# Kernel tuning notes

Hardware: AMD Instinct MI355X
Metric: run time of the kernel (lower is better)

## Reference

```python
import jax, jax.numpy as jnp
import numpy as np

N = 100000
E = 3200000
IN_F, HID_F, OUT_F = 512, 256, 64
ALPHA = 0.01
K = 10


def setup_inputs() -> dict:
    key = jax.random.key(0)
    ks = jax.random.split(key, 8)
    x = jax.random.normal(ks[0], (N, IN_F), dtype=jnp.float32)
    W1 = jax.random.normal(ks[1], (IN_F, HID_F), dtype=jnp.float32) * (1.0 / np.sqrt(IN_F))
    b1 = jnp.zeros((HID_F,), dtype=jnp.float32)
    W2 = jax.random.normal(ks[2], (HID_F, OUT_F), dtype=jnp.float32) * (1.0 / np.sqrt(HID_F))
    b2 = jnp.zeros((OUT_F,), dtype=jnp.float32)
    row = jax.random.randint(ks[3], (E,), 0, N, dtype=jnp.int32)
    col = jax.random.randint(ks[4], (E,), 0, N, dtype=jnp.int32)
    # normalized-ish positive edge weights
    edge_weight = jax.random.uniform(ks[5], (E,), dtype=jnp.float32) / 32.0
    return {"x": x, "W1": W1, "b1": b1, "W2": W2, "b2": b2,
            "edge_weight": edge_weight, "row": row, "col": col}


def _spmm(row, col, w, h):
    # sparse [N,N] @ dense [N,d]: out[r] += w_e * h[col_e]
    msgs = h[col] * w[:, None]  # [E, d]
    return jax.ops.segment_sum(msgs, row, num_segments=N)


def reference(x, W1, b1, W2, b2, edge_weight, row, col):
    h = jax.nn.relu(x @ W1 + b1)          # linear1 + activation (dropout p=0 -> identity)
    h = h @ W2 + b2                        # linear2
    for _ in range(K):                     # k-step PPR propagation, alpha-blended residual
        h = (1.0 - ALPHA) * _spmm(row, col, edge_weight, h) + ALPHA * h
    return h
```

## Files before the change

kernel.cpp:

```cpp
#include <hip/hip_runtime.h>


#define N_NODES 100000
#define N_EDGES 3200000
#define IN_F    512
#define HID_F   256
#define OUT_F   64
#define NBKT    ((N_NODES + 63) / 64)
#define CAP     4096
#define SBLK    250
#define SCHUNK  12800

typedef short bf16x8 __attribute__((ext_vector_type(8)));
typedef float f32x4  __attribute__((ext_vector_type(4)));

__device__ __forceinline__ unsigned short f2bf(float f) {
    unsigned int u = __float_as_uint(f);
    unsigned int r = (u + 0x7FFFu + ((u >> 16) & 1u)) >> 16;
    return (unsigned short)r;
}
__device__ __forceinline__ float bf2f(unsigned short h) {
    return __uint_as_float(((unsigned int)h) << 16);
}

__global__ void cast_transpose_w1(const float* __restrict__ w, unsigned short* __restrict__ wt) {
    int idx = blockIdx.x * blockDim.x + threadIdx.x;
    if (idx >= IN_F * HID_F) return;
    int k = idx / HID_F, n = idx % HID_F;
    wt[(size_t)n * IN_F + k] = f2bf(w[idx]);
}
__global__ void cast_transpose_w2(const float* __restrict__ w, unsigned short* __restrict__ wt) {
    int idx = blockIdx.x * blockDim.x + threadIdx.x;
    if (idx >= HID_F * OUT_F) return;
    int k = idx / OUT_F, n = idx % OUT_F;
    wt[(size_t)n * HID_F + k] = f2bf(w[idx]);
}

__global__ __launch_bounds__(256) void cast_x(const float* __restrict__ x,
                                              unsigned short* __restrict__ xb) {
    int idx = blockIdx.x * 256 + threadIdx.x;
    if (idx >= N_NODES * IN_F / 8) return;
    const float4* s = (const float4*)(x + (size_t)idx * 8);
    float4 f0 = s[0], f1 = s[1];
    union { bf16x8 v; unsigned short u[8]; } t;
    t.u[0] = f2bf(f0.x); t.u[1] = f2bf(f0.y); t.u[2] = f2bf(f0.z); t.u[3] = f2bf(f0.w);
    t.u[4] = f2bf(f1.x); t.u[5] = f2bf(f1.y); t.u[6] = f2bf(f1.z); t.u[7] = f2bf(f1.w);
    *(bf16x8*)(xb + (size_t)idx * 8) = t.v;
}

__global__ __launch_bounds__(512) void gemm1(const unsigned short* __restrict__ xb,
                                             const unsigned short* __restrict__ w1t,
                                             const float* __restrict__ b1,
                                             unsigned short* __restrict__ h1) {
    int tid  = threadIdx.x;
    int lane = tid & 63;
    int w    = tid >> 6;
    int wm   = w >> 2;
    int wn   = w & 3;
    int quad = lane >> 4;
    int lm   = lane & 15;
    int m0 = blockIdx.x * 64 + wm * 32;
    int n0 = wn * 64;

    f32x4 acc[2][4];
    for (int i = 0; i < 2; ++i)
        for (int j = 0; j < 4; ++j)
            acc[i][j] = (f32x4){0.f, 0.f, 0.f, 0.f};

    for (int kk = 0; kk < IN_F; kk += 32) {
        bf16x8 a[2], b[4];
        for (int i = 0; i < 2; ++i) {
            int m = m0 + i * 16 + lm;
            if (m > N_NODES - 1) m = N_NODES - 1;
            a[i] = *(const bf16x8*)(xb + (size_t)m * IN_F + kk + quad * 8);
        }
        for (int j = 0; j < 4; ++j) {
            int n = n0 + j * 16 + lm;
            b[j] = *(const bf16x8*)(w1t + (size_t)n * IN_F + kk + quad * 8);
        }
        for (int i = 0; i < 2; ++i)
            for (int j = 0; j < 4; ++j)
                acc[i][j] = __builtin_amdgcn_mfma_f32_16x16x32_bf16(a[i], b[j], acc[i][j], 0, 0, 0);
    }

    for (int i = 0; i < 2; ++i)
        for (int j = 0; j < 4; ++j) {
            int n = n0 + j * 16 + lm;
            float bias = b1[n];
            for (int r = 0; r < 4; ++r) {
                int m = m0 + i * 16 + quad * 4 + r;
                if (m < N_NODES) {
                    float v = acc[i][j][r] + bias;
                    v = v > 0.f ? v : 0.f;
                    h1[(size_t)m * HID_F + n] = f2bf(v);
                }
            }
        }
}

__global__ __launch_bounds__(256) void gemm2(const unsigned short* __restrict__ h1,
                                             const unsigned short* __restrict__ w2t,
                                             const float* __restrict__ b2,
                                             unsigned short* __restrict__ h0) {
    int tid  = threadIdx.x;
    int lane = tid & 63;
    int w    = tid >> 6;
    int wm   = w >> 1;
    int wn   = w & 1;
    int quad = lane >> 4;
    int lm   = lane & 15;
    int m0 = blockIdx.x * 64 + wm * 32;
    int n0 = wn * 32;

    f32x4 acc[2][2];
    for (int i = 0; i < 2; ++i)
        for (int j = 0; j < 2; ++j)
            acc[i][j] = (f32x4){0.f, 0.f, 0.f, 0.f};

    for (int kk = 0; kk < HID_F; kk += 32) {
        bf16x8 a[2], b[2];
        for (int i = 0; i < 2; ++i) {
            int m = m0 + i * 16 + lm;
            if (m > N_NODES - 1) m = N_NODES - 1;
            a[i] = *(const bf16x8*)(h1 + (size_t)m * HID_F + kk + quad * 8);
        }
        for (int j = 0; j < 2; ++j) {
            int n = n0 + j * 16 + lm;
            b[j] = *(const bf16x8*)(w2t + (size_t)n * HID_F + kk + quad * 8);
        }
        for (int i = 0; i < 2; ++i)
            for (int j = 0; j < 2; ++j)
                acc[i][j] = __builtin_amdgcn_mfma_f32_16x16x32_bf16(a[i], b[j], acc[i][j], 0, 0, 0);
    }

    for (int i = 0; i < 2; ++i)
        for (int j = 0; j < 2; ++j) {
            int n = n0 + j * 16 + lm;
            float bias = b2[n];
            for (int r = 0; r < 4; ++r) {
                int m = m0 + i * 16 + quad * 4 + r;
                if (m < N_NODES) {
                    float v = acc[i][j][r] + bias;
                    h0[(size_t)m * OUT_F + n] = f2bf(v);
                }
            }
        }
}

__global__ void bs_init(int* __restrict__ cur) {
    int c = blockIdx.x * blockDim.x + threadIdx.x;
    if (c < NBKT) cur[c] = c * CAP;
}

__global__ __launch_bounds__(256) void bucket_scatter(const int* __restrict__ row,
                                                      const int* __restrict__ col,
                                                      const float* __restrict__ ew,
                                                      int* __restrict__ cur,
                                                      uint2* __restrict__ tmp) {
    __shared__ int lh[NBKT];
    __shared__ int lc[NBKT];
    int tid = threadIdx.x;
    int e0 = blockIdx.x * SCHUNK;

    for (int c = tid; c < NBKT; c += 256) { lh[c] = 0; lc[c] = 0; }
    __syncthreads();
    for (int i = tid; i < SCHUNK; i += 256)
        atomicAdd(&lh[row[e0 + i] >> 6], 1);
    __syncthreads();
    for (int c = tid; c < NBKT; c += 256) {
        int n = lh[c];
        if (n) lh[c] = atomicAdd(&cur[c], n);
    }
    __syncthreads();
    for (int i = tid; i < SCHUNK; i += 256) {
        int e = e0 + i;
        int r = row[e];
        int c = r >> 6;
        int p = lh[c] + atomicAdd(&lc[c], 1);
        if (p < (c + 1) * CAP)
            tmp[p] = make_uint2((unsigned)col[e] | ((unsigned)(r & 63) << 17),
                                __float_as_uint(ew[e]));
    }
}

__global__ __launch_bounds__(64) void bkt_scan(const int* __restrict__ cur,
                                               int* __restrict__ bktbase,
                                               int* __restrict__ rowptr) {
    int lane = threadIdx.x;
    int carry = 0;
    for (int base = 0; base < NBKT; base += 64) {
        int c = base + lane;
        int v = (c < NBKT) ? (cur[c] - c * CAP) : 0;
        int incl = v;
        for (int d = 1; d < 64; d <<= 1) {
            int t = __shfl_up(incl, d);
            if (lane >= d) incl += t;
        }
        if (c < NBKT) bktbase[c] = carry + incl - v;
        carry += __shfl(incl, 63);
    }
    if (lane == 0) { bktbase[NBKT] = carry; rowptr[N_NODES] = carry; }
}

__global__ __launch_bounds__(256) void bucket_sort(const uint2* __restrict__ tmp,
                                                   const int* __restrict__ bktbase,
                                                   int* __restrict__ rowptr,
                                                   int2* __restrict__ colw) {
    __shared__ int rh[64];
    __shared__ int lcur[64];
    int c = blockIdx.x;
    int tid = threadIdx.x;
    int s = c * CAP;
    int base = bktbase[c];
    int tot = bktbase[c + 1] - base;

    if (tid < 64) rh[tid] = 0;
    __syncthreads();
    for (int i = tid; i < tot; i += 256)
        atomicAdd(&rh[(tmp[s + i].x >> 17) & 63], 1);
    __syncthreads();
    if (tid < 64) {
        int v = rh[tid];
        int incl = v;
        for (int d = 1; d < 64; d <<= 1) {
            int t = __shfl_up(incl, d);
            if (tid >= d) incl += t;
        }
        int excl = incl - v;
        int rr = c * 64 + tid;
        if (rr < N_NODES) rowptr[rr] = base + excl;
        lcur[tid] = base + excl;
    }
    __syncthreads();
    for (int i = tid; i < tot; i += 256) {
        uint2 t = tmp[s + i];
        int rl = (t.x >> 17) & 63;
        int p = atomicAdd(&lcur[rl], 1);
        colw[p] = make_int2((int)(t.x & 0x1FFFF), (int)t.y);
    }
}

__global__ __launch_bounds__(256) void prop(const unsigned short* __restrict__ hin,
                                            const int* __restrict__ rowptr,
                                            const int2* __restrict__ colw,
                                            unsigned short* __restrict__ hout,
                                            float* __restrict__ fout, int is_final) {
    int lane = threadIdx.x & 63;
    int r = blockIdx.x * 4 + (threadIdx.x >> 6);
    int fe   = lane & 7;
    int slot = lane >> 3;

    int s = rowptr[r];
    int e = rowptr[r + 1];
    const unsigned short* hfe = hin + 8 * fe;

    float af[8];
    #pragma unroll
    for (int k = 0; k < 8; ++k) af[k] = 0.f;

    int n8 = (e - s) & ~7;
    int i = s;
    #pragma unroll 2
    for (; i < s + n8; i += 8) {
        int2 cw = colw[i + slot];
        float w = __int_as_float(cw.y);
        bf16x8 p = *(const bf16x8*)(hfe + (unsigned)cw.x * (unsigned)OUT_F);
        #pragma unroll
        for (int k = 0; k < 8; ++k)
            af[k] += w * bf2f((unsigned short)p[k]);
    }
    {
        int ei = i + slot;
        if (ei < e) {
            int2 cw = colw[ei];
            float w = __int_as_float(cw.y);
            bf16x8 p = *(const bf16x8*)(hfe + (unsigned)cw.x * (unsigned)OUT_F);
            #pragma unroll
            for (int k = 0; k < 8; ++k)
                af[k] += w * bf2f((unsigned short)p[k]);
        }
    }
    #pragma unroll
    for (int k = 0; k < 8; ++k) {
        af[k] += __shfl_xor(af[k], 8);
        af[k] += __shfl_xor(af[k], 16);
        af[k] += __shfl_xor(af[k], 32);
    }

    if (slot == 0) {
        bf16x8 ps = *(const bf16x8*)(hin + (unsigned)r * (unsigned)OUT_F + 8 * fe);
        float rr[8];
        #pragma unroll
        for (int k = 0; k < 8; ++k)
            rr[k] = 0.99f * af[k] + 0.01f * bf2f((unsigned short)ps[k]);
        size_t o = (size_t)r * OUT_F + 8 * fe;
        if (is_final) {
            *(float4*)(fout + o)     = make_float4(rr[0], rr[1], rr[2], rr[3]);
            *(float4*)(fout + o + 4) = make_float4(rr[4], rr[5], rr[6], rr[7]);
        } else {
            union { bf16x8 v; unsigned short u[8]; } pk;
            #pragma unroll
            for (int k = 0; k < 8; ++k) pk.u[k] = f2bf(rr[k]);
            *(bf16x8*)(hout + o) = pk.v;
        }
    }
}

extern "C" void kernel_launch(void* const* d_in, const int* in_sizes, int n_in,
                              void* d_out, int out_size, void* d_ws, size_t ws_size,
                              hipStream_t stream) {
    (void)in_sizes; (void)n_in; (void)out_size; (void)ws_size;
    const float* x  = (const float*)d_in[0];
    const float* W1 = (const float*)d_in[1];
    const float* b1 = (const float*)d_in[2];
    const float* W2 = (const float*)d_in[3];
    const float* b2 = (const float*)d_in[4];
    const float* ew = (const float*)d_in[5];
    const int*  row = (const int*)d_in[6];
    const int*  col = (const int*)d_in[7];
    float* out = (float*)d_out;

    char* ws = (char*)d_ws;
    size_t off = 0;
    auto alloc = [&](size_t b) { char* p = ws + off; off += (b + 255) & ~(size_t)255; return p; };
    char* regionA = alloc((size_t)N_NODES * IN_F * 2);
    unsigned short* xb  = (unsigned short*)regionA;
    uint2* tmp  = (uint2*)regionA;
    int2*  colw = (int2*)(regionA + (size_t)NBKT * CAP * 8);
    unsigned short* w1t = (unsigned short*)alloc((size_t)IN_F * HID_F * 2);
    unsigned short* w2t = (unsigned short*)alloc((size_t)HID_F * OUT_F * 2);
    unsigned short* h1  = (unsigned short*)alloc((size_t)N_NODES * HID_F * 2);
    unsigned short* hb0 = (unsigned short*)alloc((size_t)N_NODES * OUT_F * 2);
    unsigned short* hb1 = (unsigned short*)alloc((size_t)N_NODES * OUT_F * 2);
    int*  rowptr  = (int*)alloc((size_t)(N_NODES + 1) * 4);
    int*  cur     = (int*)alloc((size_t)NBKT * 4);
    int*  bktbase = (int*)alloc((size_t)(NBKT + 1) * 4);

    cast_transpose_w1<<<(IN_F * HID_F + 255) / 256, 256, 0, stream>>>(W1, w1t);
    cast_transpose_w2<<<(HID_F * OUT_F + 255) / 256, 256, 0, stream>>>(W2, w2t);
    cast_x<<<(N_NODES * IN_F / 8 + 255) / 256, 256, 0, stream>>>(x, xb);
    gemm1<<<(N_NODES + 63) / 64, 512, 0, stream>>>(xb, w1t, b1, h1);
    gemm2<<<(N_NODES + 63) / 64, 256, 0, stream>>>(h1, w2t, b2, hb0);

    bs_init<<<(NBKT + 255) / 256, 256, 0, stream>>>(cur);
    bucket_scatter<<<SBLK, 256, 0, stream>>>(row, col, ew, cur, tmp);
    bkt_scan<<<1, 64, 0, stream>>>(cur, bktbase, rowptr);
    bucket_sort<<<NBKT, 256, 0, stream>>>(tmp, bktbase, rowptr, colw);

    const unsigned short* pin = hb0;
    for (int s = 0; s < 10; ++s) {
        int last = (s == 9);
        unsigned short* pout = (s & 1) ? hb0 : hb1;
        prop<<<N_NODES / 4, 256, 0, stream>>>(pin, rowptr, colw, pout, out, last);
        pin = pout;
    }
}
```

Measured before the change: 1.201 ms.

## Tile gemm1 through double-buffered LDS with 128x128 blocks

Rewrites the first GEMM to stage 128x128 tiles of A and B in padded shared memory, double-buffered, with register prefetch of the next K slice. Each wave now computes a 64x64 sub-tile (4x4 MFMAs), so each loaded fragment feeds more MFMAs. The old version loaded every fragment straight from global memory. The change adds LDS use and barriers, and raises register pressure from the larger accumulator set.

```diff
diff --git a/kernel.cpp b/kernel.cpp
--- a/kernel.cpp
+++ b/kernel.cpp
@@ -10,6 +10,11 @@
 #define CAP     4096
 #define SBLK    250
 #define SCHUNK  12800
+
+#define BM 128
+#define BN 128
+#define BK 32
+#define LDK 40
 
 typedef short bf16x8 __attribute__((ext_vector_type(8)));
 typedef float f32x4  __attribute__((ext_vector_type(4)));
@@ -48,47 +53,90 @@
     *(bf16x8*)(xb + (size_t)idx * 8) = t.v;
 }
 
-__global__ __launch_bounds__(512) void gemm1(const unsigned short* __restrict__ xb,
+__global__ __launch_bounds__(256) void gemm1(const unsigned short* __restrict__ xb,
                                              const unsigned short* __restrict__ w1t,
                                              const float* __restrict__ b1,
                                              unsigned short* __restrict__ h1) {
+    __shared__ unsigned short lA[2][BM][LDK];
+    __shared__ unsigned short lB[2][BN][LDK];
+
     int tid  = threadIdx.x;
+    int bm0  = (blockIdx.x >> 1) * BM;
+    int n0   = (blockIdx.x & 1) * BN;
     int lane = tid & 63;
     int w    = tid >> 6;
-    int wm   = w >> 2;
-    int wn   = w & 3;
+    int wm   = w >> 1;
+    int wn   = w & 1;
     int quad = lane >> 4;
     int lm   = lane & 15;
-    int m0 = blockIdx.x * 64 + wm * 32;
-    int n0 = wn * 64;
-
-    f32x4 acc[2][4];
-    for (int i = 0; i < 2; ++i)
+
+    int sr = tid >> 2;
+    int sq = (tid & 3) * 8;
+
+    f32x4 acc[4][4];
+    #pragma unroll
+    for (int i = 0; i < 4; ++i)
+        #pragma unroll
         for (int j = 0; j < 4; ++j)
             acc[i][j] = (f32x4){0.f, 0.f, 0.f, 0.f};
 
-    for (int kk = 0; kk < IN_F; kk += 32) {
-        bf16x8 a[2], b[4];
-        for (int i = 0; i < 2; ++i) {
-            int m = m0 + i * 16 + lm;
-            if (m > N_NODES - 1) m = N_NODES - 1;
-            a[i] = *(const bf16x8*)(xb + (size_t)m * IN_F + kk + quad * 8);
-        }
+    bf16x8 ra[2], rb[2];
+    #pragma unroll
+    for (int j = 0; j < 2; ++j) {
+        int m = bm0 + sr + j * 64; if (m > N_NODES - 1) m = N_NODES - 1;
+        ra[j] = *(const bf16x8*)(xb  + (size_t)m * IN_F + sq);
+        rb[j] = *(const bf16x8*)(w1t + (size_t)(n0 + sr + j * 64) * IN_F + sq);
+    }
+    #pragma unroll
+    for (int j = 0; j < 2; ++j) {
+        *(bf16x8*)&lA[0][sr + j * 64][sq] = ra[j];
+        *(bf16x8*)&lB[0][sr + j * 64][sq] = rb[j];
+    }
+    __syncthreads();
+
+    int cur = 0;
+    for (int step = 0; step < IN_F / BK; ++step) {
+        if (step + 1 < IN_F / BK) {
+            int kn = (step + 1) * BK;
+            #pragma unroll
+            for (int j = 0; j < 2; ++j) {
+                int m = bm0 + sr + j * 64; if (m > N_NODES - 1) m = N_NODES - 1;
+                ra[j] = *(const bf16x8*)(xb  + (size_t)m * IN_F + kn + sq);
+                rb[j] = *(const bf16x8*)(w1t + (size_t)(n0 + sr + j * 64) * IN_F + kn + sq);
+            }
+        }
+        bf16x8 af[4], bfr[4];
+        #pragma unroll
+        for (int i = 0; i < 4; ++i)
+            af[i] = *(const bf16x8*)&lA[cur][wm * 64 + i * 16 + lm][quad * 8];
+        #pragma unroll
+        for (int j = 0; j < 4; ++j)
+            bfr[j] = *(const bf16x8*)&lB[cur][wn * 64 + j * 16 + lm][quad * 8];
+        #pragma unroll
+        for (int i = 0; i < 4; ++i)
+            #pragma unroll
+            for (int j = 0; j < 4; ++j)
+                acc[i][j] = __builtin_amdgcn_mfma_f32_16x16x32_bf16(af[i], bfr[j], acc[i][j], 0, 0, 0);
+        if (step + 1 < IN_F / BK) {
+            #pragma unroll
+            for (int j = 0; j < 2; ++j) {
+                *(bf16x8*)&lA[cur ^ 1][sr + j * 64][sq] = ra[j];
+                *(bf16x8*)&lB[cur ^ 1][sr + j * 64][sq] = rb[j];
+            }
+            __syncthreads();
+            cur ^= 1;
+        }
+    }
+
+    #pragma unroll
+    for (int i = 0; i < 4; ++i)
+        #pragma unroll
         for (int j = 0; j < 4; ++j) {
-            int n = n0 + j * 16 + lm;
-            b[j] = *(const bf16x8*)(w1t + (size_t)n * IN_F + kk + quad * 8);
-        }
-        for (int i = 0; i < 2; ++i)
-            for (int j = 0; j < 4; ++j)
-                acc[i][j] = __builtin_amdgcn_mfma_f32_16x16x32_bf16(a[i], b[j], acc[i][j], 0, 0, 0);
-    }
-
-    for (int i = 0; i < 2; ++i)
-        for (int j = 0; j < 4; ++j) {
-            int n = n0 + j * 16 + lm;
+            int n = n0 + wn * 64 + j * 16 + lm;
             float bias = b1[n];
+            #pragma unroll
             for (int r = 0; r < 4; ++r) {
-                int m = m0 + i * 16 + quad * 4 + r;
+                int m = bm0 + wm * 64 + i * 16 + quad * 4 + r;
                 if (m < N_NODES) {
                     float v = acc[i][j][r] + bias;
                     v = v > 0.f ? v : 0.f;
@@ -339,7 +387,7 @@
     cast_transpose_w1<<<(IN_F * HID_F + 255) / 256, 256, 0, stream>>>(W1, w1t);
     cast_transpose_w2<<<(HID_F * OUT_F + 255) / 256, 256, 0, stream>>>(W2, w2t);
     cast_x<<<(N_NODES * IN_F / 8 + 255) / 256, 256, 0, stream>>>(x, xb);
-    gemm1<<<(N_NODES + 63) / 64, 512, 0, stream>>>(xb, w1t, b1, h1);
+    gemm1<<<((N_NODES + BM - 1) / BM) * 2, 256, 0, stream>>>(xb, w1t, b1, h1);
     gemm2<<<(N_NODES + 63) / 64, 256, 0, stream>>>(h1, w2t, b2, hb0);
 
     bs_init<<<(NBKT + 255) / 256, 256, 0, stream>>>(cur);
```

Measured after the change: 1.107 ms. -7.8%, faster.
